# Optimization experiments

Measured on AMD Instinct MI355X. Metric: run time of the kernel, lower is better.

The kernel has to match this reference:

```python
import jax, jax.numpy as jnp
import numpy as np
import math

B, S, D = 4, 4096, 256

def _linear(x, W, b):
    return jnp.einsum('bsd,ed->bse', x, W) + b

def _attn(x, Wq, bq, Wk, bk, Wv, bv, d):
    Q = _linear(x, Wq, bq)
    K = _linear(x, Wk, bk)
    V = _linear(x, Wv, bv)
    scores = jnp.einsum('bqd,bkd->bqk', Q, K) / math.sqrt(d)  # [B,S,S]
    w = jax.nn.softmax(scores, axis=-1)
    return jnp.einsum('bqk,bkd->bqd', w, V)

def setup_inputs() -> dict:
    key = jax.random.key(0)
    ks = jax.random.split(key, 32)
    p = {}
    p['x'] = jax.random.normal(ks[0], (B, S, D), dtype=jnp.float32)
    p['eps'] = jax.random.normal(ks[1], (B, S, D), dtype=jnp.float32)
    i = 2
    for name in ['Wq1','Wk1','Wv1','Wq2','Wk2','Wv2','Wmu','Wlv']:
        p[name] = 0.02 * jax.random.normal(ks[i], (D, D), dtype=jnp.float32); i += 1
    for name in ['bq1','bk1','bv1','bq2','bk2','bv2','bmu','blv']:
        p[name] = jnp.zeros((D,), dtype=jnp.float32)
    p['Wg'] = 0.02 * jax.random.normal(ks[i], (1, D), dtype=jnp.float32); i += 1
    p['bg'] = jnp.zeros((1,), dtype=jnp.float32)
    p['gamma'] = jnp.ones((D,), dtype=jnp.float32)
    p['beta'] = jnp.zeros((D,), dtype=jnp.float32)
    return p

def reference(x, eps, Wq1, Wk1, Wv1, Wq2, Wk2, Wv2, Wmu, Wlv,
              bq1, bk1, bv1, bq2, bk2, bv2, bmu, blv, Wg, bg, gamma, beta):
    d = x.shape[-1]
    h1 = _attn(x, Wq1, bq1, Wk1, bk1, Wv1, bv1, d)
    h2 = _attn(h1, Wq2, bq2, Wk2, bk2, Wv2, bv2, d)
    mu = _linear(h2, Wmu, bmu)
    logvar = _linear(h2, Wlv, blv)
    std = jnp.exp(0.5 * logvar)
    z = jax.nn.elu(mu + eps * std)
    p_gate = jax.nn.sigmoid(_linear(h2.mean(axis=1)[:, None, :], Wg, bg))[:, 0, 0]  # [B]
    y = x + z
    mean = y.mean(axis=-1, keepdims=True)
    var = y.var(axis=-1, keepdims=True)
    out = (y - mean) / jnp.sqrt(var + 1e-5) * gamma + beta
    return (out, mu, logvar, p_gate)
```

## Files before the change

### kernel.cpp

```cpp
#include <hip/hip_runtime.h>
#include <hip/hip_bf16.h>
#include <hip/hip_fp8.h>
#include <cstdint>
#include <cstddef>


#define S_LEN 4096
#define DMODEL 256
#define NBATCH 4
#define MTOT (NBATCH * S_LEN)

typedef __bf16 bf16;
typedef __bf16 bf16x8 __attribute__((ext_vector_type(8)));
typedef float f32x4 __attribute__((ext_vector_type(4)));
typedef float f32x16 __attribute__((ext_vector_type(16)));
typedef int i32x4 __attribute__((ext_vector_type(4)));
typedef int i32x8 __attribute__((ext_vector_type(8)));
typedef unsigned char u8;
typedef unsigned int u32;

__device__ __forceinline__ f32x4 mfma16(bf16x8 a, bf16x8 b, f32x4 c) {
  return __builtin_amdgcn_mfma_f32_16x16x32_bf16(a, b, c, 0, 0, 0);
}
__device__ __forceinline__ f32x16 mfma_mx(i32x8 a, i32x8 b, f32x16 c) {
  return __builtin_amdgcn_mfma_scale_f32_32x32x64_f8f6f4(
      a, b, c, 0 , 0 , 0, 0x7F7F7F7F, 0, 0x7F7F7F7F);
}

__device__ __forceinline__ void async16(const void* g, void* lds) {
  __builtin_amdgcn_global_load_lds(
      (const __attribute__((address_space(1))) unsigned int*)g,
      (__attribute__((address_space(3))) unsigned int*)lds, 16, 0, 0);
}

__device__ __forceinline__ unsigned short f2bfbits(float f) {
  return __builtin_bit_cast(unsigned short, (bf16)f);
}
__device__ __forceinline__ u8 f2fp8(float f) {
  __hip_fp8_e4m3 t(f);
  return *(u8*)&t;
}
__device__ __forceinline__ int permc(int v) {
  return (((v >> 5) & 1) << 7) + (((v >> 6) & 3) << 5) + (v & 31);
}

struct WPtrs { const float* p[8]; };

__global__ void cast_all_kernel(const f32x4* __restrict__ x, WPtrs wp,
                                ushort4* __restrict__ x16, ushort4* __restrict__ w16) {
  int bx = blockIdx.x, t = threadIdx.x;
  const f32x4* src;
  ushort4* dst;
  if (bx < 4096) {
    src = x + (size_t)bx * 256 + t;
    dst = x16 + (size_t)bx * 256 + t;
  } else {
    int r = bx - 4096;
    int m = r >> 6;
    int i = (r & 63) * 256 + t;
    src = (const f32x4*)wp.p[m] + i;
    dst = w16 + (size_t)m * 16384 + i;
  }
  f32x4 v = *src;
  ushort4 o;
  o.x = f2bfbits(v[0]); o.y = f2bfbits(v[1]); o.z = f2bfbits(v[2]); o.w = f2bfbits(v[3]);
  *dst = o;
}

struct GemmIO {
  const float* bias[3];
  void* out[3];
};

__global__ __launch_bounds__(256, 3) void gemm_qkv_kernel(const bf16* __restrict__ A,
                                                          const bf16* __restrict__ Wb,
                                                          GemmIO io) {
  __shared__ bf16 ldsA[128 * 64];
  __shared__ bf16 ldsB[128 * 64];
  const int t = threadIdx.x;
  const int m0 = blockIdx.x * 128;
  const int n0 = blockIdx.y * 128;
  const bf16* W = Wb + (size_t)blockIdx.z * 65536;
  const int w = t >> 6, l = t & 63, lm = l & 15, q = l >> 4;
  const int wr = (w >> 1) * 64, wc = (w & 1) * 64;

  f32x4 acc[4][4] = {};
#pragma unroll 1
  for (int it = 0; it < 4; ++it) {
    const int k0 = it * 64;
#pragma unroll
    for (int c = 0; c < 4; ++c) {
      int i = c * 256 + t;
      int r = i >> 3, c8 = (i & 7) ^ (r & 7);
      async16(A + (size_t)(m0 + r) * 256 + k0 + c8 * 8, &ldsA[i * 8]);
    }
#pragma unroll
    for (int c = 0; c < 4; ++c) {
      int i = c * 256 + t;
      int r = i >> 3, c8 = (i & 7) ^ (r & 7);
      async16(W + (size_t)(n0 + r) * 256 + k0 + c8 * 8, &ldsB[i * 8]);
    }
    __syncthreads();
#pragma unroll
    for (int ks = 0; ks < 2; ++ks) {
      bf16x8 af[4], bfr[4];
#pragma unroll
      for (int i = 0; i < 4; ++i) {
        int ra = wr + i * 16 + lm;
        af[i] = *(const bf16x8*)&ldsA[ra * 64 + ((((ks << 2) + q) ^ (ra & 7)) << 3)];
        int rb = wc + i * 16 + lm;
        bfr[i] = *(const bf16x8*)&ldsB[rb * 64 + ((((ks << 2) + q) ^ (rb & 7)) << 3)];
      }
#pragma unroll
      for (int i = 0; i < 4; ++i)
#pragma unroll
        for (int jj = 0; jj < 4; ++jj) acc[i][jj] = mfma16(af[i], bfr[jj], acc[i][jj]);
    }
    __syncthreads();
  }
  const float* bias = io.bias[blockIdx.z];
  if (blockIdx.z == 2) {
    bf16* out = (bf16*)io.out[2];
#pragma unroll
    for (int jj = 0; jj < 4; ++jj) {
      int col = n0 + wc + jj * 16 + lm;
      float bv = bias[col];
#pragma unroll
      for (int i = 0; i < 4; ++i) {
        int row = m0 + wr + i * 16 + q * 4;
#pragma unroll
        for (int r = 0; r < 4; ++r)
          out[(size_t)(row + r) * 256 + col] = (bf16)(acc[i][jj][r] + bv);
      }
    }
  } else {
    u8* out = (u8*)io.out[blockIdx.z];
#pragma unroll
    for (int jj = 0; jj < 4; ++jj) {
      int col = n0 + wc + jj * 16 + lm;
      int scol = (blockIdx.z == 1) ? permc(col) : col;
      float bv = bias[col];
#pragma unroll
      for (int i = 0; i < 4; ++i) {
        int row = m0 + wr + i * 16 + q * 4;
#pragma unroll
        for (int r = 0; r < 4; ++r)
          out[(size_t)(row + r) * 256 + scol] = f2fp8(acc[i][jj][r] + bv);
      }
    }
  }
}

__global__ __launch_bounds__(256, 3) void gemm_f_kernel(const bf16* __restrict__ A,
                                                        const bf16* __restrict__ Wb, GemmIO io) {
  __shared__ bf16 ldsA[128 * 64];
  __shared__ bf16 ldsB[128 * 64];
  const int t = threadIdx.x;
  const int m0 = blockIdx.x * 128;
  const int n0 = blockIdx.y * 128;
  const bf16* W = Wb + (size_t)blockIdx.z * 65536;
  const int w = t >> 6, l = t & 63, lm = l & 15, q = l >> 4;
  const int wr = (w >> 1) * 64, wc = (w & 1) * 64;

  f32x4 acc[4][4] = {};
#pragma unroll 1
  for (int it = 0; it < 4; ++it) {
    const int k0 = it * 64;
#pragma unroll
    for (int c = 0; c < 4; ++c) {
      int i = c * 256 + t;
      int r = i >> 3, c8 = (i & 7) ^ (r & 7);
      async16(A + (size_t)(m0 + r) * 256 + k0 + c8 * 8, &ldsA[i * 8]);
    }
#pragma unroll
    for (int c = 0; c < 4; ++c) {
      int i = c * 256 + t;
      int r = i >> 3, c8 = (i & 7) ^ (r & 7);
      async16(W + (size_t)(n0 + r) * 256 + k0 + c8 * 8, &ldsB[i * 8]);
    }
    __syncthreads();
#pragma unroll
    for (int ks = 0; ks < 2; ++ks) {
      bf16x8 af[4], bfr[4];
#pragma unroll
      for (int i = 0; i < 4; ++i) {
        int ra = wr + i * 16 + lm;
        af[i] = *(const bf16x8*)&ldsA[ra * 64 + ((((ks << 2) + q) ^ (ra & 7)) << 3)];
        int rb = wc + i * 16 + lm;
        bfr[i] = *(const bf16x8*)&ldsB[rb * 64 + ((((ks << 2) + q) ^ (rb & 7)) << 3)];
      }
#pragma unroll
      for (int i = 0; i < 4; ++i)
#pragma unroll
        for (int jj = 0; jj < 4; ++jj) acc[i][jj] = mfma16(af[i], bfr[jj], acc[i][jj]);
    }
    __syncthreads();
  }
  const float* bias = io.bias[blockIdx.z];
  float* out = (float*)io.out[blockIdx.z];
#pragma unroll
  for (int jj = 0; jj < 4; ++jj) {
    int col = n0 + wc + jj * 16 + lm;
    float bv = bias[col];
#pragma unroll
    for (int i = 0; i < 4; ++i) {
      int row = m0 + wr + i * 16 + q * 4;
#pragma unroll
      for (int r = 0; r < 4; ++r)
        out[(size_t)(row + r) * 256 + col] = acc[i][jj][r] + bv;
    }
  }
}

__global__ void transpose_kernel(const bf16* __restrict__ src, u8* __restrict__ dst) {
  __shared__ bf16 tile[64][72];
  int s0 = blockIdx.x * 64, d0 = blockIdx.y * 64;
  size_t boff = (size_t)blockIdx.z * S_LEN * 256;
  size_t boffT = (size_t)blockIdx.z * 256 * S_LEN;
  int t = threadIdx.x;
#pragma unroll
  for (int rep = 0; rep < 16; ++rep) {
    int lin = rep * 256 + t;
    int r = lin >> 6, c = lin & 63;
    tile[r][c] = src[boff + (size_t)(s0 + r) * 256 + d0 + c];
  }
  __syncthreads();
#pragma unroll
  for (int rep = 0; rep < 16; ++rep) {
    int lin = rep * 256 + t;
    int r = lin >> 6, c = lin & 63;
    int sg = s0 + c;
    int sp = (sg & ~255) + permc(sg & 255);
    dst[boffT + (size_t)(d0 + r) * S_LEN + sp] = f2fp8((float)tile[c][r]);
  }
}

__global__ __launch_bounds__(1024, 4) void flash_kernel(const u8* __restrict__ Q,
                                                        const u8* __restrict__ K,
                                                        const u8* __restrict__ Vt,
                                                        bf16* __restrict__ O) {
  __shared__ __align__(16) u8 ldsK[256 * 256];
  __shared__ __align__(16) u8 ldsV[256 * 256];
  __shared__ __align__(16) u8 ldsP[2 * 32 * 256];
  __shared__ float lb[64];

  const int id = blockIdx.x;
  const int xcd = id & 7;
  const int b = xcd >> 1;
  const int qt = (id >> 3) + ((xcd & 1) << 5);

  const u8* Qb = Q + (size_t)b * S_LEN * 256;
  const u8* Kb = K + (size_t)b * S_LEN * 256;
  const u8* Vb = Vt + (size_t)b * 256 * S_LEN;
  bf16* Ob = O + (size_t)b * S_LEN * 256;

  const int t = threadIdx.x, w = t >> 6, lane = t & 63;
  const int m31 = lane & 31, kh = lane >> 5;
  const int qg = w & 1, sub = w >> 1;
  const float CL2 = 0.09016844005556021f;

  if (t < 64) lb[t] = 0.f;

  int sld[4], skg[4], svg[4];
#pragma unroll
  for (int it = 0; it < 4; ++it) {
    int c = it * 1024 + t;
    sld[it] = c * 16;
    int kr = c >> 4, g = (c & 15) ^ (kr & 7);
    skg[it] = kr * 256 + g * 16;
    svg[it] = kr * S_LEN + g * 16;
  }
  const int kn = sub * 32 + m31;
  const u8* kbase = &ldsK[kn * 256 + kh * 128];
  const int kx = kn & 7;
  const int vd = sub * 32 + m31;
  const u8* vbase = &ldsV[vd * 256 + kh * 128];
  const int vx = vd & 7;
  const u8* pread = &ldsP[qg * 8192 + m31 * 256 + kh * 128];
  const int px = m31 & 7;
  u8* pstore = &ldsP[qg * 8192 + m31 * 256 + ((sub & 1) << 7) + 4 * kh];
  const int pc0 = (sub >> 1) << 1;

  i32x8 qf[4];
  {
    const u8* qrow = Qb + (size_t)(qt * 64 + qg * 32 + m31) * 256 + kh * 32;
#pragma unroll
    for (int b2 = 0; b2 < 4; ++b2) qf[b2] = *(const i32x8*)(qrow + b2 * 64);
  }

  f32x16 o_acc = {};
  float l_w = 0.f;

#pragma unroll
  for (int it = 0; it < 4; ++it) async16(Kb + skg[it], &ldsK[sld[it]]);

#pragma unroll 1
  for (int j = 0; j < 16; ++j) {
    __syncthreads();
    {
      const u8* vg = Vb + j * 256;
#pragma unroll
      for (int it = 0; it < 4; ++it) async16(vg + svg[it], &ldsV[sld[it]]);
    }
    f32x16 s = {};
#pragma unroll
    for (int b2 = 0; b2 < 4; ++b2) {
      i32x4 klo = *(const i32x4*)(kbase + (((2 * b2) ^ kx) << 4));
      i32x4 khi = *(const i32x4*)(kbase + (((2 * b2 + 1) ^ kx) << 4));
      i32x8 kf = __builtin_shufflevector(klo, khi, 0, 1, 2, 3, 4, 5, 6, 7);
      s = mfma_mx(kf, qf[b2], s);
    }
    float p[16];
#pragma unroll
    for (int r = 0; r < 16; ++r) {
      p[r] = __builtin_amdgcn_exp2f(s[r] * CL2);
      l_w += p[r];
    }
#pragma unroll
    for (int g2 = 0; g2 < 4; ++g2) {
      int pk = __builtin_amdgcn_cvt_pk_fp8_f32(p[4 * g2], p[4 * g2 + 1], 0, false);
      pk = __builtin_amdgcn_cvt_pk_fp8_f32(p[4 * g2 + 2], p[4 * g2 + 3], pk, true);
      *(u32*)(pstore + (((pc0 + (g2 >> 1)) ^ px) << 4) + ((g2 & 1) << 3)) = (u32)pk;
    }
    __syncthreads();
    if (j + 1 < 16) {
      const u8* kg = Kb + (size_t)(j + 1) * 65536;
#pragma unroll
      for (int it = 0; it < 4; ++it) async16(kg + skg[it], &ldsK[sld[it]]);
    }
#pragma unroll
    for (int b2 = 0; b2 < 4; ++b2) {
      i32x4 plo = *(const i32x4*)(pread + (((2 * b2) ^ px) << 4));
      i32x4 phi = *(const i32x4*)(pread + (((2 * b2 + 1) ^ px) << 4));
      i32x4 vlo = *(const i32x4*)(vbase + (((2 * b2) ^ vx) << 4));
      i32x4 vhi = *(const i32x4*)(vbase + (((2 * b2 + 1) ^ vx) << 4));
      o_acc = mfma_mx(__builtin_shufflevector(plo, phi, 0, 1, 2, 3, 4, 5, 6, 7),
                      __builtin_shufflevector(vlo, vhi, 0, 1, 2, 3, 4, 5, 6, 7), o_acc);
    }
  }

  l_w += __shfl_xor(l_w, 32, 64);
  if (kh == 0) atomicAdd(&lb[qg * 32 + m31], l_w);
  __syncthreads();

  bf16* orow = Ob + (size_t)(qt * 64 + qg * 32) * 256 + sub * 32;
#pragma unroll
  for (int reg = 0; reg < 16; ++reg) {
    const int row = (reg & 3) + 8 * (reg >> 2) + 4 * kh;
    orow[(size_t)row * 256 + m31] = (bf16)(o_acc[reg] / lb[qg * 32 + row]);
  }
}

__global__ __launch_bounds__(256) void gate_partial(const bf16* __restrict__ h,
                                                    float* __restrict__ part) {
  int bb = blockIdx.y;
  const bf16* hb = h + (size_t)bb * S_LEN * 256 + (size_t)blockIdx.x * 64 * 256;
  int t = threadIdx.x;
  float acc = 0.f;
#pragma unroll 4
  for (int s = 0; s < 64; ++s) acc += (float)hb[s * 256 + t];
  part[((size_t)bb * 64 + blockIdx.x) * 256 + t] = acc;
}

__global__ __launch_bounds__(256) void gate_final(const float* __restrict__ part,
                                                  const float* __restrict__ Wg,
                                                  const float* __restrict__ bg,
                                                  float* __restrict__ pg) {
  int bb = blockIdx.x, t = threadIdx.x;
  const float* p = part + (size_t)bb * 64 * 256;
  float acc = 0.f;
#pragma unroll 4
  for (int c = 0; c < 64; ++c) acc += p[c * 256 + t];
  acc *= Wg[t] * (1.0f / 4096.0f);
  __shared__ float red[256];
  red[t] = acc;
  __syncthreads();
  if (t < 64) {
    float a = red[t] + red[t + 64] + red[t + 128] + red[t + 192];
#pragma unroll
    for (int d = 1; d < 64; d <<= 1) a += __shfl_xor(a, d, 64);
    if (t == 0) pg[bb] = 1.0f / (1.0f + __expf(-(a + bg[0])));
  }
}

__global__ __launch_bounds__(256) void epilogue_kernel(const float* __restrict__ x,
                                                       const float* __restrict__ eps,
                                                       const float* __restrict__ mu,
                                                       const float* __restrict__ lv,
                                                       const float* __restrict__ gamma,
                                                       const float* __restrict__ beta,
                                                       float* __restrict__ out) {
  size_t base = (size_t)blockIdx.x * 1024 + (threadIdx.x >> 6) * 256;
  int l = threadIdx.x & 63;
  f32x4 xv = ((const f32x4*)(x + base))[l];
  f32x4 ev = ((const f32x4*)(eps + base))[l];
  f32x4 mv = ((const f32x4*)(mu + base))[l];
  f32x4 vv = ((const f32x4*)(lv + base))[l];
  f32x4 y;
  float s = 0.f, s2 = 0.f;
#pragma unroll
  for (int c = 0; c < 4; ++c) {
    float z = mv[c] + ev[c] * __expf(0.5f * vv[c]);
    z = z > 0.f ? z : (__expf(z) - 1.f);
    float yy = xv[c] + z;
    y[c] = yy;
    s += yy;
    s2 += yy * yy;
  }
#pragma unroll
  for (int d = 1; d < 64; d <<= 1) {
    s += __shfl_xor(s, d, 64);
    s2 += __shfl_xor(s2, d, 64);
  }
  float mean = s * (1.f / 256.f);
  float var = s2 * (1.f / 256.f) - mean * mean;
  float rstd = rsqrtf(var + 1e-5f);
  f32x4 gv = ((const f32x4*)gamma)[l];
  f32x4 bv = ((const f32x4*)beta)[l];
  f32x4 o;
#pragma unroll
  for (int c = 0; c < 4; ++c) o[c] = (y[c] - mean) * rstd * gv[c] + bv[c];
  ((f32x4*)(out + base))[l] = o;
}

extern "C" void kernel_launch(void* const* d_in, const int* in_sizes, int n_in, void* d_out,
                              int out_size, void* d_ws, size_t ws_size, hipStream_t stream) {
  const float* x = (const float*)d_in[0];
  const float* eps = (const float*)d_in[1];
  const float* Wg = (const float*)d_in[18];
  const float* bg = (const float*)d_in[19];
  const float* gamma = (const float*)d_in[20];
  const float* beta = (const float*)d_in[21];

  char* ws = (char*)d_ws;
  bf16* x16 = (bf16*)(ws);
  bf16* h16 = (bf16*)(ws + 8388608);
  bf16* v16 = (bf16*)(ws + 16777216);
  u8* q8 = (u8*)(ws + 25165824);
  u8* k8 = (u8*)(ws + 29360128);
  u8* vt8 = (u8*)(ws + 33554432);
  bf16* w16 = (bf16*)(ws + 37748736);
  float* gpart = (float*)(ws + 38797312);

  float* out = (float*)d_out;
  float* mu = out + 4194304;
  float* lv = out + 8388608;
  float* pg = out + 12582912;

  WPtrs wp;
  for (int i = 0; i < 8; ++i) wp.p[i] = (const float*)d_in[2 + i];
  cast_all_kernel<<<4608, 256, 0, stream>>>((const f32x4*)x, wp, (ushort4*)x16, (ushort4*)w16);

  GemmIO io1;
  io1.bias[0] = (const float*)d_in[10];
  io1.bias[1] = (const float*)d_in[11];
  io1.bias[2] = (const float*)d_in[12];
  io1.out[0] = q8; io1.out[1] = k8; io1.out[2] = v16;
  gemm_qkv_kernel<<<dim3(128, 2, 3), 256, 0, stream>>>(x16, w16, io1);
  transpose_kernel<<<dim3(64, 4, 4), 256, 0, stream>>>(v16, vt8);
  flash_kernel<<<256, 1024, 0, stream>>>(q8, k8, vt8, h16);

  GemmIO io2;
  io2.bias[0] = (const float*)d_in[13];
  io2.bias[1] = (const float*)d_in[14];
  io2.bias[2] = (const float*)d_in[15];
  io2.out[0] = q8; io2.out[1] = k8; io2.out[2] = v16;
  gemm_qkv_kernel<<<dim3(128, 2, 3), 256, 0, stream>>>(h16, w16 + 3 * 65536, io2);
  transpose_kernel<<<dim3(64, 4, 4), 256, 0, stream>>>(v16, vt8);
  flash_kernel<<<256, 1024, 0, stream>>>(q8, k8, vt8, h16);

  GemmIO io3;
  io3.bias[0] = (const float*)d_in[16];
  io3.bias[1] = (const float*)d_in[17];
  io3.bias[2] = nullptr;
  io3.out[0] = mu; io3.out[1] = lv; io3.out[2] = nullptr;
  gemm_f_kernel<<<dim3(128, 2, 2), 256, 0, stream>>>(h16, w16 + 6 * 65536, io3);

  gate_partial<<<dim3(64, 4), 256, 0, stream>>>(h16, gpart);
  gate_final<<<4, 256, 0, stream>>>(gpart, Wg, bg, pg);
  epilogue_kernel<<<4096, 256, 0, stream>>>(x, eps, mu, lv, gamma, beta, out);
}
```

Baseline: 285.7 us.

## Warp-specialize flash kernel into QK/softmax producers and PV consumers with double buffering

The flash attention kernel's 16 waves are split into two roles. Eight producer waves compute QK^T scores and exp into fp8 P tiles. Eight consumer waves run the P·V MFMAs one step behind, with K, V and P held in double-buffered LDS over half-size 128-key tiles. The V transpose permutation changes to match the 128-key tile layout, and s_setprio is raised around the MFMA sections. The aim is to overlap softmax and PV work and to drop one barrier per iteration, at the cost of twice as many iterations and barriers and possible idle time if the two roles are unbalanced.

```diff
diff --git a/kernel.cpp b/kernel.cpp
--- a/kernel.cpp
+++ b/kernel.cpp
@@ -42,6 +42,9 @@
 }
 __device__ __forceinline__ int permc(int v) {
   return (((v >> 5) & 1) << 7) + (((v >> 6) & 3) << 5) + (v & 31);
+}
+__device__ __forceinline__ int permc128(int v) {
+  return (((v >> 5) & 1) << 6) + (((v >> 6) & 1) << 5) + (v & 31);
 }
 
 struct WPtrs { const float* p[8]; };
@@ -230,7 +233,7 @@
     int lin = rep * 256 + t;
     int r = lin >> 6, c = lin & 63;
     int sg = s0 + c;
-    int sp = (sg & ~255) + permc(sg & 255);
+    int sp = (sg & ~127) + permc128(sg & 127);
     dst[boffT + (size_t)(d0 + r) * S_LEN + sp] = f2fp8((float)tile[c][r]);
   }
 }
@@ -239,9 +242,9 @@
                                                         const u8* __restrict__ K,
                                                         const u8* __restrict__ Vt,
                                                         bf16* __restrict__ O) {
-  __shared__ __align__(16) u8 ldsK[256 * 256];
-  __shared__ __align__(16) u8 ldsV[256 * 256];
-  __shared__ __align__(16) u8 ldsP[2 * 32 * 256];
+  __shared__ __align__(16) u8 ldsK[2][128 * 256];
+  __shared__ __align__(16) u8 ldsV[2][256 * 128];
+  __shared__ __align__(16) u8 ldsP[2][2 * 32 * 128];
   __shared__ float lb[64];
 
   const int id = blockIdx.x;
@@ -256,98 +259,125 @@
 
   const int t = threadIdx.x, w = t >> 6, lane = t & 63;
   const int m31 = lane & 31, kh = lane >> 5;
-  const int qg = w & 1, sub = w >> 1;
+  const bool prod = (w < 8);
   const float CL2 = 0.09016844005556021f;
 
   if (t < 64) lb[t] = 0.f;
 
-  int sld[4], skg[4], svg[4];
-#pragma unroll
-  for (int it = 0; it < 4; ++it) {
+  int kld[2], kgo[2], vld[2], vgo[2];
+#pragma unroll
+  for (int it = 0; it < 2; ++it) {
     int c = it * 1024 + t;
-    sld[it] = c * 16;
-    int kr = c >> 4, g = (c & 15) ^ (kr & 7);
-    skg[it] = kr * 256 + g * 16;
-    svg[it] = kr * S_LEN + g * 16;
-  }
-  const int kn = sub * 32 + m31;
-  const u8* kbase = &ldsK[kn * 256 + kh * 128];
+    kld[it] = c * 16;
+    int kr = c >> 4, kg2 = (c & 15) ^ (kr & 7);
+    kgo[it] = kr * 256 + kg2 * 16;
+    vld[it] = c * 16;
+    int vr = c >> 3, vg2 = (c & 7) ^ (vr & 7);
+    vgo[it] = vr * S_LEN + vg2 * 16;
+  }
+
+  const int qg = w & 1, ks = (w >> 1) & 3;
+  const int kn = ks * 32 + m31;
   const int kx = kn & 7;
-  const int vd = sub * 32 + m31;
-  const u8* vbase = &ldsV[vd * 256 + kh * 128];
-  const int vx = vd & 7;
-  const u8* pread = &ldsP[qg * 8192 + m31 * 256 + kh * 128];
   const int px = m31 & 7;
-  u8* pstore = &ldsP[qg * 8192 + m31 * 256 + ((sub & 1) << 7) + 4 * kh];
-  const int pc0 = (sub >> 1) << 1;
-
   i32x8 qf[4];
-  {
+  if (prod) {
     const u8* qrow = Qb + (size_t)(qt * 64 + qg * 32 + m31) * 256 + kh * 32;
 #pragma unroll
     for (int b2 = 0; b2 < 4; ++b2) qf[b2] = *(const i32x8*)(qrow + b2 * 64);
   }
-
-  f32x16 o_acc = {};
+  const int cw = w - 8;
+  const int cqg = cw & 1, dpair = cw >> 1;
+  const int vd0 = dpair * 64 + m31;
+  const int vx = vd0 & 7;
+
+  f32x16 o0 = {}, o1 = {};
   float l_w = 0.f;
 
 #pragma unroll
-  for (int it = 0; it < 4; ++it) async16(Kb + skg[it], &ldsK[sld[it]]);
+  for (int it = 0; it < 2; ++it) async16(Kb + kgo[it], &ldsK[0][kld[it]]);
+  __syncthreads();
 
 #pragma unroll 1
-  for (int j = 0; j < 16; ++j) {
+  for (int j = 0; j <= 32; ++j) {
+    if (j < 32) {
+      const u8* vg = Vb + j * 128;
+#pragma unroll
+      for (int it = 0; it < 2; ++it) async16(vg + vgo[it], &ldsV[j & 1][vld[it]]);
+    }
+    if (j < 31) {
+      const u8* kg = Kb + (size_t)(j + 1) * 128 * 256;
+#pragma unroll
+      for (int it = 0; it < 2; ++it) async16(kg + kgo[it], &ldsK[(j + 1) & 1][kld[it]]);
+    }
+    if (prod) {
+      if (j < 32) {
+        const u8* kb = &ldsK[j & 1][kn * 256 + kh * 128];
+        f32x16 s = {};
+        __builtin_amdgcn_s_setprio(1);
+#pragma unroll
+        for (int b2 = 0; b2 < 4; ++b2) {
+          i32x4 klo = *(const i32x4*)(kb + (((2 * b2) ^ kx) << 4));
+          i32x4 khi = *(const i32x4*)(kb + (((2 * b2 + 1) ^ kx) << 4));
+          s = mfma_mx(__builtin_shufflevector(klo, khi, 0, 1, 2, 3, 4, 5, 6, 7), qf[b2], s);
+        }
+        __builtin_amdgcn_s_setprio(0);
+        float p[16];
+#pragma unroll
+        for (int r = 0; r < 16; ++r) {
+          p[r] = __builtin_amdgcn_exp2f(s[r] * CL2);
+          l_w += p[r];
+        }
+        u8* pst = &ldsP[j & 1][qg * 4096 + m31 * 128 + 4 * kh];
+        const int cb = (ks & 1) * 4 + (ks >> 1) * 2;
+#pragma unroll
+        for (int g2 = 0; g2 < 4; ++g2) {
+          int pk = __builtin_amdgcn_cvt_pk_fp8_f32(p[4 * g2], p[4 * g2 + 1], 0, false);
+          pk = __builtin_amdgcn_cvt_pk_fp8_f32(p[4 * g2 + 2], p[4 * g2 + 3], pk, true);
+          *(u32*)(pst + (((cb + (g2 >> 1)) ^ px) << 4) + ((g2 & 1) << 3)) = (u32)pk;
+        }
+      }
+    } else {
+      if (j > 0) {
+        const int pb = (j - 1) & 1;
+        const u8* pr = &ldsP[pb][cqg * 4096 + m31 * 128];
+        const u8* v0 = &ldsV[pb][(size_t)vd0 * 128];
+        const u8* v1 = v0 + 32 * 128;
+        __builtin_amdgcn_s_setprio(1);
+#pragma unroll
+        for (int b2 = 0; b2 < 2; ++b2) {
+          const int ca = 4 * kh + 2 * b2;
+          i32x4 plo = *(const i32x4*)(pr + ((ca ^ px) << 4));
+          i32x4 phi = *(const i32x4*)(pr + (((ca + 1) ^ px) << 4));
+          i32x8 pa = __builtin_shufflevector(plo, phi, 0, 1, 2, 3, 4, 5, 6, 7);
+          i32x4 va = *(const i32x4*)(v0 + ((ca ^ vx) << 4));
+          i32x4 vb2 = *(const i32x4*)(v0 + (((ca + 1) ^ vx) << 4));
+          o0 = mfma_mx(pa, __builtin_shufflevector(va, vb2, 0, 1, 2, 3, 4, 5, 6, 7), o0);
+          i32x4 vc = *(const i32x4*)(v1 + ((ca ^ vx) << 4));
+          i32x4 vd2 = *(const i32x4*)(v1 + (((ca + 1) ^ vx) << 4));
+          o1 = mfma_mx(pa, __builtin_shufflevector(vc, vd2, 0, 1, 2, 3, 4, 5, 6, 7), o1);
+        }
+        __builtin_amdgcn_s_setprio(0);
+      }
+    }
     __syncthreads();
-    {
-      const u8* vg = Vb + j * 256;
-#pragma unroll
-      for (int it = 0; it < 4; ++it) async16(vg + svg[it], &ldsV[sld[it]]);
-    }
-    f32x16 s = {};
-#pragma unroll
-    for (int b2 = 0; b2 < 4; ++b2) {
-      i32x4 klo = *(const i32x4*)(kbase + (((2 * b2) ^ kx) << 4));
-      i32x4 khi = *(const i32x4*)(kbase + (((2 * b2 + 1) ^ kx) << 4));
-      i32x8 kf = __builtin_shufflevector(klo, khi, 0, 1, 2, 3, 4, 5, 6, 7);
-      s = mfma_mx(kf, qf[b2], s);
-    }
-    float p[16];
-#pragma unroll
-    for (int r = 0; r < 16; ++r) {
-      p[r] = __builtin_amdgcn_exp2f(s[r] * CL2);
-      l_w += p[r];
-    }
-#pragma unroll
-    for (int g2 = 0; g2 < 4; ++g2) {
-      int pk = __builtin_amdgcn_cvt_pk_fp8_f32(p[4 * g2], p[4 * g2 + 1], 0, false);
-      pk = __builtin_amdgcn_cvt_pk_fp8_f32(p[4 * g2 + 2], p[4 * g2 + 3], pk, true);
-      *(u32*)(pstore + (((pc0 + (g2 >> 1)) ^ px) << 4) + ((g2 & 1) << 3)) = (u32)pk;
-    }
-    __syncthreads();
-    if (j + 1 < 16) {
-      const u8* kg = Kb + (size_t)(j + 1) * 65536;
-#pragma unroll
-      for (int it = 0; it < 4; ++it) async16(kg + skg[it], &ldsK[sld[it]]);
-    }
-#pragma unroll
-    for (int b2 = 0; b2 < 4; ++b2) {
-      i32x4 plo = *(const i32x4*)(pread + (((2 * b2) ^ px) << 4));
-      i32x4 phi = *(const i32x4*)(pread + (((2 * b2 + 1) ^ px) << 4));
-      i32x4 vlo = *(const i32x4*)(vbase + (((2 * b2) ^ vx) << 4));
-      i32x4 vhi = *(const i32x4*)(vbase + (((2 * b2 + 1) ^ vx) << 4));
-      o_acc = mfma_mx(__builtin_shufflevector(plo, phi, 0, 1, 2, 3, 4, 5, 6, 7),
-                      __builtin_shufflevector(vlo, vhi, 0, 1, 2, 3, 4, 5, 6, 7), o_acc);
-    }
-  }
-
-  l_w += __shfl_xor(l_w, 32, 64);
-  if (kh == 0) atomicAdd(&lb[qg * 32 + m31], l_w);
+  }
+
+  if (prod) {
+    l_w += __shfl_xor(l_w, 32, 64);
+    if (kh == 0) atomicAdd(&lb[qg * 32 + m31], l_w);
+  }
   __syncthreads();
 
-  bf16* orow = Ob + (size_t)(qt * 64 + qg * 32) * 256 + sub * 32;
-#pragma unroll
-  for (int reg = 0; reg < 16; ++reg) {
-    const int row = (reg & 3) + 8 * (reg >> 2) + 4 * kh;
-    orow[(size_t)row * 256 + m31] = (bf16)(o_acc[reg] / lb[qg * 32 + row]);
+  if (!prod) {
+    bf16* ob0 = Ob + (size_t)(qt * 64 + cqg * 32) * 256 + dpair * 64;
+#pragma unroll
+    for (int reg = 0; reg < 16; ++reg) {
+      const int row = (reg & 3) + 8 * (reg >> 2) + 4 * kh;
+      float li = lb[cqg * 32 + row];
+      ob0[(size_t)row * 256 + m31] = (bf16)(o0[reg] / li);
+      ob0[(size_t)row * 256 + 32 + m31] = (bf16)(o1[reg] / li);
+    }
   }
 }
 
```

Result: slower. 298.2 us (+4.4%).

## Warp-specialize flash attention with producer/consumer pipeline and fuse V transpose into GEMM

Applied to the files above, without the earlier changes.

The QKV GEMM now writes V directly as fp8 in a blocked transposed layout, so the separate transpose kernel and the bf16 V buffer are no longer needed. The flash kernel is rewritten with 32-query blocks and 384 threads. Two producer waves compute QK^T and softmax probabilities into a double-buffered P tile. Four consumer waves load V straight from global memory into registers, stage K tiles into a 4-deep LDS ring, and run the PV MFMAs one step behind the producers. The aim is to overlap score computation with PV and memory loads, and to cut LDS footprint and barriers per tile, at the cost of extra raw s_barrier synchronization and less MFMA parallelism per block.

```diff
diff --git a/kernel.cpp b/kernel.cpp
--- a/kernel.cpp
+++ b/kernel.cpp
@@ -8,7 +8,6 @@
 #define S_LEN 4096
 #define DMODEL 256
 #define NBATCH 4
-#define MTOT (NBATCH * S_LEN)
 
 typedef __bf16 bf16;
 typedef __bf16 bf16x8 __attribute__((ext_vector_type(8)));
@@ -24,7 +23,10 @@
 }
 __device__ __forceinline__ f32x16 mfma_mx(i32x8 a, i32x8 b, f32x16 c) {
   return __builtin_amdgcn_mfma_scale_f32_32x32x64_f8f6f4(
-      a, b, c, 0 , 0 , 0, 0x7F7F7F7F, 0, 0x7F7F7F7F);
+      a, b, c, 0, 0, 0, 0x7F7F7F7F, 0, 0x7F7F7F7F);
+}
+__device__ __forceinline__ i32x8 cat8(i32x4 a, i32x4 b) {
+  return __builtin_shufflevector(a, b, 0, 1, 2, 3, 4, 5, 6, 7);
 }
 
 __device__ __forceinline__ void async16(const void* g, void* lds) {
@@ -120,7 +122,7 @@
   }
   const float* bias = io.bias[blockIdx.z];
   if (blockIdx.z == 2) {
-    bf16* out = (bf16*)io.out[2];
+    u8* out = (u8*)io.out[2];
 #pragma unroll
     for (int jj = 0; jj < 4; ++jj) {
       int col = n0 + wc + jj * 16 + lm;
@@ -129,8 +131,12 @@
       for (int i = 0; i < 4; ++i) {
         int row = m0 + wr + i * 16 + q * 4;
 #pragma unroll
-        for (int r = 0; r < 4; ++r)
-          out[(size_t)(row + r) * 256 + col] = (bf16)(acc[i][jj][r] + bv);
+        for (int r = 0; r < 4; ++r) {
+          int rg = row + r;
+          int bb = rg >> 12, s = rg & 4095;
+          out[(((size_t)(bb * 64 + (s >> 6)) * 256 + col) << 6) + (s & 63)] =
+              f2fp8(acc[i][jj][r] + bv);
+        }
       }
     }
   } else {
@@ -212,142 +218,182 @@
   }
 }
 
-__global__ void transpose_kernel(const bf16* __restrict__ src, u8* __restrict__ dst) {
-  __shared__ bf16 tile[64][72];
-  int s0 = blockIdx.x * 64, d0 = blockIdx.y * 64;
-  size_t boff = (size_t)blockIdx.z * S_LEN * 256;
-  size_t boffT = (size_t)blockIdx.z * 256 * S_LEN;
-  int t = threadIdx.x;
-#pragma unroll
-  for (int rep = 0; rep < 16; ++rep) {
-    int lin = rep * 256 + t;
-    int r = lin >> 6, c = lin & 63;
-    tile[r][c] = src[boff + (size_t)(s0 + r) * 256 + d0 + c];
-  }
-  __syncthreads();
-#pragma unroll
-  for (int rep = 0; rep < 16; ++rep) {
-    int lin = rep * 256 + t;
-    int r = lin >> 6, c = lin & 63;
-    int sg = s0 + c;
-    int sp = (sg & ~255) + permc(sg & 255);
-    dst[boffT + (size_t)(d0 + r) * S_LEN + sp] = f2fp8((float)tile[c][r]);
-  }
-}
-
-__global__ __launch_bounds__(1024, 4) void flash_kernel(const u8* __restrict__ Q,
-                                                        const u8* __restrict__ K,
-                                                        const u8* __restrict__ Vt,
-                                                        bf16* __restrict__ O) {
-  __shared__ __align__(16) u8 ldsK[256 * 256];
-  __shared__ __align__(16) u8 ldsV[256 * 256];
-  __shared__ __align__(16) u8 ldsP[2 * 32 * 256];
-  __shared__ float lb[64];
+__global__ __launch_bounds__(384, 3) void flash_kernel(const u8* __restrict__ Q,
+                                                       const u8* __restrict__ K,
+                                                       const u8* __restrict__ Vt,
+                                                       bf16* __restrict__ O) {
+  __shared__ __align__(16) u8 ldsK[4][16384];
+  __shared__ __align__(16) u8 ldsP[2][32 * 80];
+  __shared__ float lb[32];
 
   const int id = blockIdx.x;
   const int xcd = id & 7;
   const int b = xcd >> 1;
-  const int qt = (id >> 3) + ((xcd & 1) << 5);
+  const int qt = (id >> 3) + ((xcd & 1) << 6);
 
   const u8* Qb = Q + (size_t)b * S_LEN * 256;
   const u8* Kb = K + (size_t)b * S_LEN * 256;
-  const u8* Vb = Vt + (size_t)b * 256 * S_LEN;
+  const u8* Vb = Vt + (size_t)b * 64 * 16384;
   bf16* Ob = O + (size_t)b * S_LEN * 256;
 
   const int t = threadIdx.x, w = t >> 6, lane = t & 63;
   const int m31 = lane & 31, kh = lane >> 5;
-  const int qg = w & 1, sub = w >> 1;
+  const bool prod = (w < 2);
   const float CL2 = 0.09016844005556021f;
 
-  if (t < 64) lb[t] = 0.f;
-
-  int sld[4], skg[4], svg[4];
-#pragma unroll
-  for (int it = 0; it < 4; ++it) {
-    int c = it * 1024 + t;
-    sld[it] = c * 16;
-    int kr = c >> 4, g = (c & 15) ^ (kr & 7);
-    skg[it] = kr * 256 + g * 16;
-    svg[it] = kr * S_LEN + g * 16;
-  }
-  const int kn = sub * 32 + m31;
-  const u8* kbase = &ldsK[kn * 256 + kh * 128];
-  const int kx = kn & 7;
-  const int vd = sub * 32 + m31;
-  const u8* vbase = &ldsV[vd * 256 + kh * 128];
-  const int vx = vd & 7;
-  const u8* pread = &ldsP[qg * 8192 + m31 * 256 + kh * 128];
-  const int px = m31 & 7;
-  u8* pstore = &ldsP[qg * 8192 + m31 * 256 + ((sub & 1) << 7) + 4 * kh];
-  const int pc0 = (sub >> 1) << 1;
-
+  if (t < 32) lb[t] = 0.f;
+
+  const int ks = w & 1;
+  const int kn = ks * 32 + m31;
+  const int kx = m31 & 7;
   i32x8 qf[4];
-  {
-    const u8* qrow = Qb + (size_t)(qt * 64 + qg * 32 + m31) * 256 + kh * 32;
+  if (prod) {
+    const u8* qrow = Qb + (size_t)(qt * 32 + m31) * 256 + kh * 32;
 #pragma unroll
     for (int b2 = 0; b2 < 4; ++b2) qf[b2] = *(const i32x8*)(qrow + b2 * 64);
   }
-
-  f32x16 o_acc = {};
   float l_w = 0.f;
 
-#pragma unroll
-  for (int it = 0; it < 4; ++it) async16(Kb + skg[it], &ldsK[sld[it]]);
-
-#pragma unroll 1
-  for (int j = 0; j < 16; ++j) {
-    __syncthreads();
+  const int dpair = w - 2;
+  const int vd0 = dpair * 64 + m31;
+  const int cl = dpair * 64 + lane;
+  f32x16 o0 = {}, o1 = {};
+  i32x4 vA[4], vB[4];
+
+  auto STAGE = [&](int m) {
+    const u8* kg = Kb + (size_t)m * 16384;
+    u8* kd = ldsK[m & 3];
+#pragma unroll
+    for (int jj = 0; jj < 4; ++jj) {
+      int c = jj * 256 + cl;
+      int kr = c >> 4, g = (c & 15) ^ (kr & 7);
+      async16(kg + kr * 256 + g * 16, kd + c * 16);
+    }
+  };
+  auto CONSV = [&](int m, i32x4* vr) {
+    const u8* vt = Vb + (size_t)m * 16384 + (size_t)vd0 * 64 + kh * 32;
+    vr[0] = *(const i32x4*)(vt);
+    vr[1] = *(const i32x4*)(vt + 16);
+    vr[2] = *(const i32x4*)(vt + 2048);
+    vr[3] = *(const i32x4*)(vt + 2064);
+  };
+  auto PROD = [&](int i) {
+    const u8* kb = &ldsK[i & 3][kn * 256 + kh * 128];
+    f32x16 sA = {}, sB = {};
     {
-      const u8* vg = Vb + j * 256;
-#pragma unroll
-      for (int it = 0; it < 4; ++it) async16(vg + svg[it], &ldsV[sld[it]]);
-    }
-    f32x16 s = {};
-#pragma unroll
-    for (int b2 = 0; b2 < 4; ++b2) {
-      i32x4 klo = *(const i32x4*)(kbase + (((2 * b2) ^ kx) << 4));
-      i32x4 khi = *(const i32x4*)(kbase + (((2 * b2 + 1) ^ kx) << 4));
-      i32x8 kf = __builtin_shufflevector(klo, khi, 0, 1, 2, 3, 4, 5, 6, 7);
-      s = mfma_mx(kf, qf[b2], s);
+      i32x4 c0 = *(const i32x4*)(kb + ((0 ^ kx) << 4));
+      i32x4 c1 = *(const i32x4*)(kb + ((1 ^ kx) << 4));
+      sA = mfma_mx(cat8(c0, c1), qf[0], sA);
+      i32x4 c2 = *(const i32x4*)(kb + ((2 ^ kx) << 4));
+      i32x4 c3 = *(const i32x4*)(kb + ((3 ^ kx) << 4));
+      sB = mfma_mx(cat8(c2, c3), qf[1], sB);
+      i32x4 c4 = *(const i32x4*)(kb + ((4 ^ kx) << 4));
+      i32x4 c5 = *(const i32x4*)(kb + ((5 ^ kx) << 4));
+      sA = mfma_mx(cat8(c4, c5), qf[2], sA);
+      i32x4 c6 = *(const i32x4*)(kb + ((6 ^ kx) << 4));
+      i32x4 c7 = *(const i32x4*)(kb + ((7 ^ kx) << 4));
+      sB = mfma_mx(cat8(c6, c7), qf[3], sB);
     }
     float p[16];
+    float l0 = 0.f, l1 = 0.f, l2 = 0.f, l3 = 0.f;
 #pragma unroll
     for (int r = 0; r < 16; ++r) {
-      p[r] = __builtin_amdgcn_exp2f(s[r] * CL2);
-      l_w += p[r];
-    }
+      p[r] = __builtin_amdgcn_exp2f((sA[r] + sB[r]) * CL2);
+      if ((r & 3) == 0) l0 += p[r];
+      else if ((r & 3) == 1) l1 += p[r];
+      else if ((r & 3) == 2) l2 += p[r];
+      else l3 += p[r];
+    }
+    l_w += (l0 + l1) + (l2 + l3);
+    u8* pst = &ldsP[i & 1][m31 * 80 + ks * 32 + 4 * kh];
 #pragma unroll
     for (int g2 = 0; g2 < 4; ++g2) {
       int pk = __builtin_amdgcn_cvt_pk_fp8_f32(p[4 * g2], p[4 * g2 + 1], 0, false);
       pk = __builtin_amdgcn_cvt_pk_fp8_f32(p[4 * g2 + 2], p[4 * g2 + 3], pk, true);
-      *(u32*)(pstore + (((pc0 + (g2 >> 1)) ^ px) << 4) + ((g2 & 1) << 3)) = (u32)pk;
-    }
-    __syncthreads();
-    if (j + 1 < 16) {
-      const u8* kg = Kb + (size_t)(j + 1) * 65536;
-#pragma unroll
-      for (int it = 0; it < 4; ++it) async16(kg + skg[it], &ldsK[sld[it]]);
-    }
-#pragma unroll
-    for (int b2 = 0; b2 < 4; ++b2) {
-      i32x4 plo = *(const i32x4*)(pread + (((2 * b2) ^ px) << 4));
-      i32x4 phi = *(const i32x4*)(pread + (((2 * b2 + 1) ^ px) << 4));
-      i32x4 vlo = *(const i32x4*)(vbase + (((2 * b2) ^ vx) << 4));
-      i32x4 vhi = *(const i32x4*)(vbase + (((2 * b2 + 1) ^ vx) << 4));
-      o_acc = mfma_mx(__builtin_shufflevector(plo, phi, 0, 1, 2, 3, 4, 5, 6, 7),
-                      __builtin_shufflevector(vlo, vhi, 0, 1, 2, 3, 4, 5, 6, 7), o_acc);
-    }
-  }
-
-  l_w += __shfl_xor(l_w, 32, 64);
-  if (kh == 0) atomicAdd(&lb[qg * 32 + m31], l_w);
+      *(u32*)(pst + 8 * g2) = (u32)pk;
+    }
+  };
+  auto PV = [&](int i, const i32x4* vr) {
+    const u8* pr = &ldsP[i & 1][m31 * 80 + kh * 32];
+    i32x4 plo = *(const i32x4*)(pr);
+    i32x4 phi = *(const i32x4*)(pr + 16);
+    i32x8 pa = cat8(plo, phi);
+    o0 = mfma_mx(pa, cat8(vr[0], vr[1]), o0);
+    o1 = mfma_mx(pa, cat8(vr[2], vr[3]), o1);
+  };
+
+#pragma unroll
+  for (int rep = 0; rep < 8; ++rep) {
+    int c = rep * 384 + t;
+    int tile = c >> 10, cc = c & 1023;
+    int kr = cc >> 4, g = (cc & 15) ^ (kr & 7);
+    async16(Kb + tile * 16384 + kr * 256 + g * 16, &ldsK[tile][cc * 16]);
+  }
+  asm volatile("s_waitcnt vmcnt(0) lgkmcnt(0)" ::: "memory");
+  __builtin_amdgcn_s_barrier();
+  asm volatile("" ::: "memory");
+
+  if (prod) {
+    PROD(0);
+    asm volatile("s_waitcnt lgkmcnt(0)" ::: "memory");
+  } else {
+    CONSV(0, vA);
+    STAGE(3);
+  }
+  __builtin_amdgcn_s_barrier();
+  asm volatile("" ::: "memory");
+
+#pragma unroll 1
+  for (int ii = 1; ii < 63; ii += 2) {
+    if (prod) {
+      PROD(ii);
+      asm volatile("s_waitcnt lgkmcnt(0)" ::: "memory");
+    } else {
+      CONSV(ii, vB);
+      if (ii + 3 < 64) STAGE(ii + 3);
+      PV(ii - 1, vA);
+    }
+    __builtin_amdgcn_s_barrier();
+    asm volatile("" ::: "memory");
+    if (prod) {
+      PROD(ii + 1);
+      asm volatile("s_waitcnt lgkmcnt(0)" ::: "memory");
+    } else {
+      CONSV(ii + 1, vA);
+      if (ii + 4 < 64) STAGE(ii + 4);
+      PV(ii, vB);
+    }
+    __builtin_amdgcn_s_barrier();
+    asm volatile("" ::: "memory");
+  }
+
+  if (prod) {
+    PROD(63);
+    asm volatile("s_waitcnt lgkmcnt(0)" ::: "memory");
+  } else {
+    CONSV(63, vB);
+    PV(62, vA);
+  }
+  __builtin_amdgcn_s_barrier();
+  asm volatile("" ::: "memory");
+
+  if (prod) {
+    l_w += __shfl_xor(l_w, 32, 64);
+    if (kh == 0) atomicAdd(&lb[m31], l_w);
+  } else {
+    PV(63, vB);
+  }
   __syncthreads();
 
-  bf16* orow = Ob + (size_t)(qt * 64 + qg * 32) * 256 + sub * 32;
-#pragma unroll
-  for (int reg = 0; reg < 16; ++reg) {
-    const int row = (reg & 3) + 8 * (reg >> 2) + 4 * kh;
-    orow[(size_t)row * 256 + m31] = (bf16)(o_acc[reg] / lb[qg * 32 + row]);
+  if (!prod) {
+    bf16* ob = Ob + (size_t)(qt * 32) * 256 + dpair * 64;
+#pragma unroll
+    for (int reg = 0; reg < 16; ++reg) {
+      const int row = (reg & 3) + 8 * (reg >> 2) + 4 * kh;
+      float li = lb[row];
+      ob[(size_t)row * 256 + m31] = (bf16)(o0[reg] / li);
+      ob[(size_t)row * 256 + 32 + m31] = (bf16)(o1[reg] / li);
+    }
   }
 }
 
@@ -435,7 +481,6 @@
   char* ws = (char*)d_ws;
   bf16* x16 = (bf16*)(ws);
   bf16* h16 = (bf16*)(ws + 8388608);
-  bf16* v16 = (bf16*)(ws + 16777216);
   u8* q8 = (u8*)(ws + 25165824);
   u8* k8 = (u8*)(ws + 29360128);
   u8* vt8 = (u8*)(ws + 33554432);
@@ -455,19 +500,17 @@
   io1.bias[0] = (const float*)d_in[10];
   io1.bias[1] = (const float*)d_in[11];
   io1.bias[2] = (const float*)d_in[12];
-  io1.out[0] = q8; io1.out[1] = k8; io1.out[2] = v16;
+  io1.out[0] = q8; io1.out[1] = k8; io1.out[2] = vt8;
   gemm_qkv_kernel<<<dim3(128, 2, 3), 256, 0, stream>>>(x16, w16, io1);
-  transpose_kernel<<<dim3(64, 4, 4), 256, 0, stream>>>(v16, vt8);
-  flash_kernel<<<256, 1024, 0, stream>>>(q8, k8, vt8, h16);
+  flash_kernel<<<512, 384, 0, stream>>>(q8, k8, vt8, h16);
 
   GemmIO io2;
   io2.bias[0] = (const float*)d_in[13];
   io2.bias[1] = (const float*)d_in[14];
   io2.bias[2] = (const float*)d_in[15];
-  io2.out[0] = q8; io2.out[1] = k8; io2.out[2] = v16;
+  io2.out[0] = q8; io2.out[1] = k8; io2.out[2] = vt8;
   gemm_qkv_kernel<<<dim3(128, 2, 3), 256, 0, stream>>>(h16, w16 + 3 * 65536, io2);
-  transpose_kernel<<<dim3(64, 4, 4), 256, 0, stream>>>(v16, vt8);
-  flash_kernel<<<256, 1024, 0, stream>>>(q8, k8, vt8, h16);
+  flash_kernel<<<512, 384, 0, stream>>>(q8, k8, vt8, h16);
 
   GemmIO io3;
   io3.bias[0] = (const float*)d_in[16];
```

New measurement: 458.5 us. 60.5% more time.
